# Performance work log

Measured on AMD Instinct MI355X. Metric: run time of the kernel, lower is better.

Reference implementation:

```python
import jax, jax.numpy as jnp
import numpy as np

B, C, H, W = 16, 256, 64, 64
HID, N, SD, NH, HD, NC = 256, 300, 64, 4, 16, 80


def _conv1x1(x, w, b):
    # x: (B,Cin,H,W), w: (Cout,Cin)
    return jnp.einsum('bchw,oc->bohw', x, w) + b[None, :, None, None]


def _lin(x, w, b):
    return x @ w.T + b


def _ln(x, g, b, eps=1e-5):
    mu = x.mean(-1, keepdims=True)
    var = ((x - mu) ** 2).mean(-1, keepdims=True)
    return (x - mu) / jnp.sqrt(var + eps) * g + b


def setup_inputs() -> dict:
    key = jax.random.key(0)
    ks = jax.random.split(key, 16)
    def w(k, shape, s=0.02):
        return jax.random.normal(k, shape, jnp.float32) * s
    return {
        'x': jax.random.normal(ks[0], (B, C, H, W), jnp.float32),
        'spotlight_sources': w(ks[1], (N, SD)),
        'pos_w': w(ks[2], (HID // 2, 2)), 'pos_b': jnp.zeros((HID // 2,), jnp.float32),
        'fp_w': w(ks[3], (HID, C)), 'fp_b': jnp.zeros((HID,), jnp.float32),
        'bn_g': jnp.ones((HID,), jnp.float32), 'bn_b': jnp.zeros((HID,), jnp.float32),
        'bn_m': jnp.zeros((HID,), jnp.float32), 'bn_v': jnp.ones((HID,), jnp.float32),
        'key_w': w(ks[4], (SD, HID)), 'key_b': jnp.zeros((SD,), jnp.float32),
        'val_w': w(ks[5], (HID, HID)), 'val_b': jnp.zeros((HID,), jnp.float32),
        'ctp_w': w(ks[6], (NC, HID)), 'ctp_b': jnp.zeros((NC,), jnp.float32),
        'bb1_w': w(ks[7], (HID, HID)), 'bb1_b': jnp.zeros((HID,), jnp.float32),
        'bbln_g': jnp.ones((HID,), jnp.float32), 'bbln_b': jnp.zeros((HID,), jnp.float32),
        'bb2_w': w(ks[8], (HID // 2, HID)), 'bb2_b': jnp.zeros((HID // 2,), jnp.float32),
        'bb3_w': w(ks[9], (4, HID // 2)), 'bb3_b': jnp.zeros((4,), jnp.float32),
        'ch1_w': w(ks[10], (HID, HID)), 'ch1_b': jnp.zeros((HID,), jnp.float32),
        'chln_g': jnp.ones((HID,), jnp.float32), 'chln_b': jnp.zeros((HID,), jnp.float32),
        'ch2_w': w(ks[11], (HID // 2, HID)), 'ch2_b': jnp.zeros((HID // 2,), jnp.float32),
        'ch3_w': w(ks[12], (1, HID // 2)), 'ch3_b': jnp.zeros((1,), jnp.float32),
    }


def _forward(x, spotlight_sources, pos_w, pos_b, fp_w, fp_b, bn_g, bn_b, bn_m, bn_v,
             key_w, key_b, val_w, val_b, ctp_w, ctp_b,
             bb1_w, bb1_b, bbln_g, bbln_b, bb2_w, bb2_b, bb3_w, bb3_b,
             ch1_w, ch1_b, chln_g, chln_b, ch2_w, ch2_b, ch3_w, ch3_b):
    Bv, _, Hh, Ww = x.shape
    # position encoding: 2-channel normalized (y, x) grid, conv1x1 to HID//2
    y = jnp.linspace(-1.0, 1.0, Hh, dtype=jnp.float32)
    xc = jnp.linspace(-1.0, 1.0, Ww, dtype=jnp.float32)
    coords = jnp.stack([jnp.broadcast_to(y[:, None], (Hh, Ww)),
                        jnp.broadcast_to(xc[None, :], (Hh, Ww))], 0)[None]  # (1,2,H,W)
    # feature_proj: conv1x1 + BatchNorm(eval) + ReLU
    feats = _conv1x1(x, fp_w, fp_b)
    feats = (feats - bn_m[None, :, None, None]) / jnp.sqrt(bn_v[None, :, None, None] + 1e-5)
    feats = jax.nn.relu(feats * bn_g[None, :, None, None] + bn_b[None, :, None, None])
    pos = jnp.broadcast_to(_conv1x1(coords, pos_w, pos_b), (Bv, HID // 2, Hh, Ww))
    comb = jnp.concatenate([feats[:, :HID // 2], pos], axis=1)  # (B,HID,H,W)
    keys = _conv1x1(comb, key_w, key_b).reshape(Bv, NH, HD, Hh * Ww)   # (B,h,d,M)
    vals = _conv1x1(comb, val_w, val_b).reshape(Bv, HID, Hh * Ww)      # (B,HID,M)
    q = spotlight_sources.reshape(N, NH, HD)                            # (N,h,d)
    logits = jnp.einsum('nhd,bhdm->bhnm', q, keys) / jnp.sqrt(jnp.float32(HD))
    attn = jax.nn.softmax(logits, axis=-1).mean(axis=1)                 # (B,N,M), head-averaged
    maps = attn.reshape(Bv, N, Hh, Ww)
    sf = jnp.einsum('bnm,bcm->bnc', attn, vals)                         # (B,N,HID)
    def head(z, w1, b1, g, bb, w2, b2, w3, b3):
        z = jax.nn.relu(_ln(_lin(z, w1, b1), g, bb))
        z = jax.nn.relu(_lin(z, w2, b2))
        return _lin(z, w3, b3)
    boxes = head(sf, bb1_w, bb1_b, bbln_g, bbln_b, bb2_w, bb2_b, bb3_w, bb3_b)
    scores = jax.nn.sigmoid(head(sf, ch1_w, ch1_b, chln_g, chln_b, ch2_w, ch2_b, ch3_w, ch3_b))
    cls = _lin(sf, ctp_w, ctp_b)
    # diversity loss: mean off-diagonal cosine similarity of attention rows
    an = attn / jnp.maximum(jnp.linalg.norm(attn, axis=2, keepdims=True), 1e-12)
    sim = jnp.einsum('bnm,bkm->bnk', an, an)
    div = (sim.sum() - jnp.einsum('bnn->', sim)) / (N * (N - 1)) * 0.1
    return boxes, scores, cls, maps, div, sf


def reference(x, spotlight_sources, pos_w, pos_b, fp_w, fp_b, bn_g, bn_b, bn_m, bn_v,
              key_w, key_b, val_w, val_b, ctp_w, ctp_b,
              bb1_w, bb1_b, bbln_g, bbln_b, bb2_w, bb2_b, bb3_w, bb3_b,
              ch1_w, ch1_b, chln_g, chln_b, ch2_w, ch2_b, ch3_w, ch3_b):
    return _forward(x, spotlight_sources, pos_w, pos_b, fp_w, fp_b, bn_g, bn_b, bn_m, bn_v,
                    key_w, key_b, val_w, val_b, ctp_w, ctp_b,
                    bb1_w, bb1_b, bbln_g, bbln_b, bb2_w, bb2_b, bb3_w, bb3_b,
                    ch1_w, ch1_b, chln_g, chln_b, ch2_w, ch2_b, ch3_w, ch3_b)
```

## Files before the change

kernel.cpp:

```cpp
#include <hip/hip_runtime.h>
#include <math.h>

#define BB 16
#define CIN 256
#define MM 4096
#define HIDC 256
#define NQ 300
#define NHH 4
#define HDD 16

#define OFF_BOXES  0
#define OFF_SCORES 19200
#define OFF_CLS    24000
#define OFF_MAPS   408000
#define OFF_DIV    20068800
#define OFF_SF     20068801

#define WS_COMB16  0
#define WS_KEYS16  8388608
#define WS_ATTN16  10485760
#define WS_T32     20316160
#define WS_T16     21544960
#define WS_VALW16  22159360
#define WS_SUMS    22192128
#define WS_NORM    22211328
#define WS_ACC     22216128
#define WS_P       22216192

#define HP_SF16   (WS_P + 0)
#define HP_Z1PRE  (WS_P + 614400)
#define HP_Z1_16  (WS_P + 1843200)
#define HP_Z2BB   (WS_P + 2457600)
#define HP_Z2CH   (WS_P + 2764800)
#define HP_HW     (WS_P + 3072000)
#define WS_Q16    (WS_P + 3200000)

#define HW_BB1 0
#define HW_CH1 65536
#define HW_BB2 131072
#define HW_CH2 163840
#define HW_CTP 196608

typedef short short8 __attribute__((ext_vector_type(8)));
typedef float floatx4 __attribute__((ext_vector_type(4)));

__device__ __forceinline__ unsigned short f2bf(float f){
  unsigned int u = __float_as_uint(f);
  u = (u + 0x7FFFu + ((u >> 16) & 1u)) >> 16;
  return (unsigned short)u;
}
__device__ __forceinline__ float bf1(unsigned short u){
  return __uint_as_float((unsigned int)u << 16);
}
__device__ __forceinline__ float4 ld_bf4(const unsigned short* p){
  ushort4 u = *(const ushort4*)p;
  float4 f;
  f.x = bf1(u.x); f.y = bf1(u.y); f.z = bf1(u.z); f.w = bf1(u.w);
  return f;
}

__global__ void zero_kernel(float* p){ p[0] = 0.f; }

__global__ __launch_bounds__(256) void zero4_kernel(float4* __restrict__ p, int n4){
  int i = blockIdx.x * 256 + threadIdx.x;
  if (i < n4) p[i] = make_float4(0.f, 0.f, 0.f, 0.f);
}

__global__ __launch_bounds__(256) void cast4_bf16_kernel(const float* __restrict__ src,
                                                         unsigned short* __restrict__ dst, int n4){
  int i = blockIdx.x * 256 + threadIdx.x;
  if (i < n4){
    float4 v = ((const float4*)src)[i];
    ushort4 u;
    u.x = f2bf(v.x); u.y = f2bf(v.y); u.z = f2bf(v.z); u.w = f2bf(v.w);
    ((ushort4*)dst)[i] = u;
  }
}

__global__ __launch_bounds__(256) void castq_kernel(const float* __restrict__ ss,
                                                    unsigned short* __restrict__ q16){
  int i = blockIdx.x * 256 + threadIdx.x;
  if (i < 320*64)
    q16[i] = (i < NQ*64) ? f2bf(ss[i] * 0.25f) : (unsigned short)0;
}

__global__ __launch_bounds__(256) void cast_heads_kernel(
    const float* __restrict__ val_w, const float* __restrict__ bb1_w,
    const float* __restrict__ ch1_w, const float* __restrict__ bb2_w,
    const float* __restrict__ ch2_w, const float* __restrict__ ctp_w,
    unsigned short* __restrict__ valw16, unsigned short* __restrict__ hw16){
  int i = blockIdx.x * 256 + threadIdx.x;
  int T = gridDim.x * 256;
  for (int j = i; j < 65536; j += T) valw16[j] = f2bf(val_w[j]);
  for (int j = i; j < 65536; j += T) hw16[HW_BB1 + j] = f2bf(bb1_w[j]);
  for (int j = i; j < 65536; j += T) hw16[HW_CH1 + j] = f2bf(ch1_w[j]);
  for (int j = i; j < 32768; j += T) hw16[HW_BB2 + j] = f2bf(bb2_w[j]);
  for (int j = i; j < 32768; j += T) hw16[HW_CH2 + j] = f2bf(ch2_w[j]);
  for (int j = i; j < 20480; j += T) hw16[HW_CTP + j] = f2bf(ctp_w[j]);
}

__global__ __launch_bounds__(256) void pos_fill_kernel(const float* __restrict__ pos_w,
                                                       const float* __restrict__ pos_b,
                                                       unsigned short* __restrict__ comb16){
  int idx = blockIdx.x * 256 + threadIdx.x;
  int c = idx >> 12;
  int m = idx & 4095;
  int row = m >> 6, col = m & 63;
  float y = -1.f + 2.f * (float)row / 63.f;
  float x = -1.f + 2.f * (float)col / 63.f;
  unsigned short v = f2bf(pos_w[c*2] * y + pos_w[c*2+1] * x + pos_b[c]);
  #pragma unroll
  for (int b = 0; b < BB; b++)
    comb16[((size_t)(b*HIDC + 128 + c))*MM + m] = v;
}

__global__ __launch_bounds__(256) void comb_gemm_kernel(const float* __restrict__ x,
    const float* __restrict__ fp_w, const float* __restrict__ fp_b,
    const float* __restrict__ bn_g, const float* __restrict__ bn_b,
    const float* __restrict__ bn_m, const float* __restrict__ bn_v,
    unsigned short* __restrict__ comb16){
  int b = blockIdx.z;
  int col0 = blockIdx.x * 128;
  const float* xb = x + (size_t)b * CIN * MM;
  unsigned short* cb = comb16 + (size_t)b * HIDC * MM;
  __shared__ float as[16][132];
  __shared__ float bs[16][128];
  int tx = threadIdx.x, ty = threadIdx.y;
  int tid = ty * 16 + tx;
  float acc[8][8] = {};
  for (int k0 = 0; k0 < CIN; k0 += 16){
    {
      int r = tid >> 1, kh = (tid & 1) * 8;
      float4 v0 = *(const float4*)&fp_w[(size_t)r * CIN + k0 + kh];
      float4 v1 = *(const float4*)&fp_w[(size_t)r * CIN + k0 + kh + 4];
      as[kh+0][r] = v0.x; as[kh+1][r] = v0.y; as[kh+2][r] = v0.z; as[kh+3][r] = v0.w;
      as[kh+4][r] = v1.x; as[kh+5][r] = v1.y; as[kh+6][r] = v1.z; as[kh+7][r] = v1.w;
    }
    {
      int kk = tid >> 4, j = (tid & 15) * 8;
      *(float4*)&bs[kk][j]     = *(const float4*)&xb[(size_t)(k0 + kk) * MM + col0 + j];
      *(float4*)&bs[kk][j + 4] = *(const float4*)&xb[(size_t)(k0 + kk) * MM + col0 + j + 4];
    }
    __syncthreads();
    #pragma unroll
    for (int kk = 0; kk < 16; kk++){
      float4 a0 = *(const float4*)&as[kk][ty*8];
      float4 a1 = *(const float4*)&as[kk][ty*8 + 4];
      float4 b0 = *(const float4*)&bs[kk][tx*8];
      float4 b1 = *(const float4*)&bs[kk][tx*8 + 4];
      float av[8] = {a0.x,a0.y,a0.z,a0.w,a1.x,a1.y,a1.z,a1.w};
      float bv[8] = {b0.x,b0.y,b0.z,b0.w,b1.x,b1.y,b1.z,b1.w};
      #pragma unroll
      for (int i = 0; i < 8; i++)
        #pragma unroll
        for (int j = 0; j < 8; j++)
          acc[i][j] += av[i] * bv[j];
    }
    __syncthreads();
  }
  #pragma unroll
  for (int i = 0; i < 8; i++){
    int r = ty*8 + i;
    float sc = rsqrtf(bn_v[r] + 1e-5f);
    float bias = fp_b[r], mu = bn_m[r], g = bn_g[r], bt = bn_b[r];
    ushort4 o0, o1;
    float v;
    v = fmaxf((acc[i][0] + bias - mu) * sc * g + bt, 0.f); o0.x = f2bf(v);
    v = fmaxf((acc[i][1] + bias - mu) * sc * g + bt, 0.f); o0.y = f2bf(v);
    v = fmaxf((acc[i][2] + bias - mu) * sc * g + bt, 0.f); o0.z = f2bf(v);
    v = fmaxf((acc[i][3] + bias - mu) * sc * g + bt, 0.f); o0.w = f2bf(v);
    v = fmaxf((acc[i][4] + bias - mu) * sc * g + bt, 0.f); o1.x = f2bf(v);
    v = fmaxf((acc[i][5] + bias - mu) * sc * g + bt, 0.f); o1.y = f2bf(v);
    v = fmaxf((acc[i][6] + bias - mu) * sc * g + bt, 0.f); o1.z = f2bf(v);
    v = fmaxf((acc[i][7] + bias - mu) * sc * g + bt, 0.f); o1.w = f2bf(v);
    *(ushort4*)&cb[(size_t)r * MM + col0 + tx*8]     = o0;
    *(ushort4*)&cb[(size_t)r * MM + col0 + tx*8 + 4] = o1;
  }
}

__global__ __launch_bounds__(256) void keys_gemm_kernel(const unsigned short* __restrict__ comb16,
    const float* __restrict__ key_w, const float* __restrict__ key_b,
    unsigned short* __restrict__ keysT){
  int b = blockIdx.z;
  int col0 = blockIdx.x * 128;
  const unsigned short* cb = comb16 + (size_t)b * HIDC * MM;
  unsigned short* kbT = keysT + (size_t)b * MM * 64;
  __shared__ float as[16][68];
  __shared__ float bs[16][132];
  int tx = threadIdx.x, ty = threadIdx.y;
  int tid = ty * 16 + tx;
  float acc[4][8] = {};
  for (int k0 = 0; k0 < HIDC; k0 += 16){
    {
      int r = tid >> 2, kh = (tid & 3) * 4;
      float4 v0 = *(const float4*)&key_w[(size_t)r * HIDC + k0 + kh];
      as[kh+0][r] = v0.x; as[kh+1][r] = v0.y; as[kh+2][r] = v0.z; as[kh+3][r] = v0.w;
    }
    {
      int kk = tid >> 4, j = (tid & 15) * 8;
      float4 f0 = ld_bf4(&cb[(size_t)(k0 + kk) * MM + col0 + j]);
      float4 f1 = ld_bf4(&cb[(size_t)(k0 + kk) * MM + col0 + j + 4]);
      *(float4*)&bs[kk][j]     = f0;
      *(float4*)&bs[kk][j + 4] = f1;
    }
    __syncthreads();
    #pragma unroll
    for (int kk = 0; kk < 16; kk++){
      float4 a0 = *(const float4*)&as[kk][ty*4];
      float4 b0 = *(const float4*)&bs[kk][tx*8];
      float4 b1 = *(const float4*)&bs[kk][tx*8 + 4];
      float av[4] = {a0.x,a0.y,a0.z,a0.w};
      float bv[8] = {b0.x,b0.y,b0.z,b0.w,b1.x,b1.y,b1.z,b1.w};
      #pragma unroll
      for (int i = 0; i < 4; i++)
        #pragma unroll
        for (int j = 0; j < 8; j++)
          acc[i][j] += av[i] * bv[j];
    }
    __syncthreads();
  }
  float kb0 = key_b[ty*4+0], kb1 = key_b[ty*4+1], kb2 = key_b[ty*4+2], kb3 = key_b[ty*4+3];
  #pragma unroll
  for (int j = 0; j < 8; j++){
    int m = col0 + tx*8 + j;
    ushort4 o;
    o.x = f2bf(acc[0][j] + kb0);
    o.y = f2bf(acc[1][j] + kb1);
    o.z = f2bf(acc[2][j] + kb2);
    o.w = f2bf(acc[3][j] + kb3);
    *(ushort4*)&kbT[(size_t)m*64 + ty*4] = o;
  }
}


__global__ __launch_bounds__(256) void attn_sums_kernel(
    const unsigned short* __restrict__ q16, const unsigned short* __restrict__ keysT,
    float* __restrict__ sums){
  int b = blockIdx.z, ny = blockIdx.y, mx = blockIdx.x;
  int tid = threadIdx.x, w = tid >> 6, lane = tid & 63;
  int n0 = ny * 64;
  int l15 = lane & 15, qh = lane >> 4;
  int ko = (qh & 1) * 8;
  bool lo = lane < 32;
  const unsigned short* kT = keysT + (size_t)b * MM * 64;
  int mwb = mx*512 + w*128;
  __shared__ float spart[4][NHH][64];
  short8 zz = {0,0,0,0,0,0,0,0};
  for (int h = 0; h < NHH; h++){
    short8 a[4];
    #pragma unroll
    for (int i = 0; i < 4; i++)
      a[i] = lo ? *(const short8*)&q16[(size_t)(n0 + i*16 + l15)*64 + h*16 + ko] : zz;
    floatx4 sacc[4];
    #pragma unroll
    for (int i = 0; i < 4; i++) sacc[i] = (floatx4){0.f,0.f,0.f,0.f};
    for (int ms = 0; ms < 8; ms++){
      int m = mwb + ms*16 + l15;
      short8 bf = lo ? *(const short8*)&kT[(size_t)m*64 + h*16 + ko] : zz;
      #pragma unroll
      for (int i = 0; i < 4; i++){
        floatx4 l = __builtin_amdgcn_mfma_f32_16x16x32_bf16(a[i], bf,
                        (floatx4){0.f,0.f,0.f,0.f}, 0, 0, 0);
        sacc[i][0] += __expf(l[0]); sacc[i][1] += __expf(l[1]);
        sacc[i][2] += __expf(l[2]); sacc[i][3] += __expf(l[3]);
      }
    }
    #pragma unroll
    for (int i = 0; i < 4; i++)
      #pragma unroll
      for (int reg = 0; reg < 4; reg++){
        float v = sacc[i][reg];
        v += __shfl_xor(v, 1); v += __shfl_xor(v, 2);
        v += __shfl_xor(v, 4); v += __shfl_xor(v, 8);
        if (l15 == 0) spart[w][h][i*16 + qh*4 + reg] = v;
      }
  }
  __syncthreads();
  if (tid < NHH*64){
    int h = tid >> 6, r = tid & 63, n = n0 + r;
    if (n < NQ){
      float v = spart[0][h][r] + spart[1][h][r] + spart[2][h][r] + spart[3][h][r];
      atomicAdd(&sums[((size_t)b*NHH + h)*NQ + n], v);
    }
  }
}

__global__ __launch_bounds__(256) void attn_emit_kernel(
    const unsigned short* __restrict__ q16, const unsigned short* __restrict__ keysT,
    const float* __restrict__ sums, float* __restrict__ maps,
    unsigned short* __restrict__ attn16, float* __restrict__ norms){
  int b = blockIdx.z, ny = blockIdx.y, mx = blockIdx.x;
  int tid = threadIdx.x, w = tid >> 6, lane = tid & 63;
  int n0 = ny * 64;
  int l15 = lane & 15, qh = lane >> 4;
  int ko = (qh & 1) * 8;
  int rq = qh * 4;
  bool lo = lane < 32;
  __shared__ __align__(16) float inv_s[NHH][64];
  __shared__ float npart[4][64];
  if (tid < NHH*64){
    int h = tid >> 6, r = tid & 63, n = n0 + r;
    inv_s[h][r] = (n < NQ) ? 0.25f / sums[((size_t)b*NHH + h)*NQ + n] : 0.f;
  }
  __syncthreads();
  const unsigned short* kT = keysT + (size_t)b * MM * 64;
  int mwb = mx*512 + w*128;
  short8 zz = {0,0,0,0,0,0,0,0};
  short8 a[NHH][4];
  #pragma unroll
  for (int h = 0; h < NHH; h++)
    #pragma unroll
    for (int i = 0; i < 4; i++)
      a[h][i] = lo ? *(const short8*)&q16[(size_t)(n0 + i*16 + l15)*64 + h*16 + ko] : zz;
  floatx4 nacc[4];
  #pragma unroll
  for (int i = 0; i < 4; i++) nacc[i] = (floatx4){0.f,0.f,0.f,0.f};
  float* mb = maps + (size_t)b * NQ * MM;
  unsigned short* ab = attn16 + (size_t)b * NQ * MM;
  for (int ms = 0; ms < 8; ms++){
    int m = mwb + ms*16 + l15;
    floatx4 o[4];
    #pragma unroll
    for (int i = 0; i < 4; i++) o[i] = (floatx4){0.f,0.f,0.f,0.f};
    #pragma unroll
    for (int h = 0; h < NHH; h++){
      short8 bf = lo ? *(const short8*)&kT[(size_t)m*64 + h*16 + ko] : zz;
      #pragma unroll
      for (int i = 0; i < 4; i++){
        floatx4 l = __builtin_amdgcn_mfma_f32_16x16x32_bf16(a[h][i], bf,
                        (floatx4){0.f,0.f,0.f,0.f}, 0, 0, 0);
        floatx4 iv = *(const floatx4*)&inv_s[h][i*16 + rq];
        o[i][0] += __expf(l[0]) * iv[0];
        o[i][1] += __expf(l[1]) * iv[1];
        o[i][2] += __expf(l[2]) * iv[2];
        o[i][3] += __expf(l[3]) * iv[3];
      }
    }
    #pragma unroll
    for (int i = 0; i < 4; i++){
      nacc[i][0] += o[i][0]*o[i][0]; nacc[i][1] += o[i][1]*o[i][1];
      nacc[i][2] += o[i][2]*o[i][2]; nacc[i][3] += o[i][3]*o[i][3];
      #pragma unroll
      for (int reg = 0; reg < 4; reg++){
        int n = n0 + i*16 + rq + reg;
        if (n < NQ){
          mb[(size_t)n*MM + m] = o[i][reg];
          ab[(size_t)n*MM + m] = f2bf(o[i][reg]);
        }
      }
    }
  }
  #pragma unroll
  for (int i = 0; i < 4; i++)
    #pragma unroll
    for (int reg = 0; reg < 4; reg++){
      float v = nacc[i][reg];
      v += __shfl_xor(v, 1); v += __shfl_xor(v, 2);
      v += __shfl_xor(v, 4); v += __shfl_xor(v, 8);
      if (l15 == 0) npart[w][i*16 + rq + reg] = v;
    }
  __syncthreads();
  if (tid < 64){
    int n = n0 + tid;
    if (n < NQ){
      float v = npart[0][tid] + npart[1][tid] + npart[2][tid] + npart[3][tid];
      atomicAdd(&norms[(size_t)b*NQ + n], v);
    }
  }
}

template<bool RELU>
__global__ __launch_bounds__(64) void mfma_nt_kernel(
    const unsigned short* __restrict__ A, size_t sA,
    const unsigned short* __restrict__ B, size_t sB,
    const float* __restrict__ bias,
    float* __restrict__ C, unsigned short* __restrict__ C16,
    size_t sC, int ldc, int Mr, int Nc, int K){
  int bz = blockIdx.z;
  const unsigned short* Ab = A + (size_t)bz * sA;
  const unsigned short* Bb = B + (size_t)bz * sB;
  int lane = threadIdx.x;
  int r16 = lane & 15;
  int ko  = (lane >> 4) * 8;
  const unsigned short* arow[4];
  const unsigned short* brow[4];
  #pragma unroll
  for (int i = 0; i < 4; i++){
    int m = blockIdx.y*64 + i*16 + r16;
    if (m > Mr - 1) m = Mr - 1;
    arow[i] = Ab + (size_t)m * K + ko;
    int n = blockIdx.x*64 + i*16 + r16;
    if (n > Nc - 1) n = Nc - 1;
    brow[i] = Bb + (size_t)n * K + ko;
  }
  floatx4 acc[4][4];
  #pragma unroll
  for (int i = 0; i < 4; i++)
    #pragma unroll
    for (int j = 0; j < 4; j++)
      acc[i][j] = (floatx4){0.f, 0.f, 0.f, 0.f};
  short8 a[4], bv[4], a2[4], b2[4];
  #pragma unroll
  for (int i = 0; i < 4; i++){
    a[i]  = *(const short8*)(arow[i]);
    bv[i] = *(const short8*)(brow[i]);
  }
  for (int k = 32; k < K; k += 32){
    #pragma unroll
    for (int i = 0; i < 4; i++){
      a2[i] = *(const short8*)(arow[i] + k);
      b2[i] = *(const short8*)(brow[i] + k);
    }
    #pragma unroll
    for (int i = 0; i < 4; i++)
      #pragma unroll
      for (int j = 0; j < 4; j++)
        acc[i][j] = __builtin_amdgcn_mfma_f32_16x16x32_bf16(a[i], bv[j], acc[i][j], 0, 0, 0);
    #pragma unroll
    for (int i = 0; i < 4; i++){ a[i] = a2[i]; bv[i] = b2[i]; }
  }
  #pragma unroll
  for (int i = 0; i < 4; i++)
    #pragma unroll
    for (int j = 0; j < 4; j++)
      acc[i][j] = __builtin_amdgcn_mfma_f32_16x16x32_bf16(a[i], bv[j], acc[i][j], 0, 0, 0);
  int cq = lane & 15, rq = (lane >> 4) * 4;
  #pragma unroll
  for (int j = 0; j < 4; j++){
    int cc = blockIdx.x*64 + j*16 + cq;
    if (cc >= Nc) continue;
    float bv_ = bias ? bias[cc] : 0.f;
    #pragma unroll
    for (int i = 0; i < 4; i++){
      int rbase = blockIdx.y*64 + i*16 + rq;
      #pragma unroll
      for (int reg = 0; reg < 4; reg++){
        int rr = rbase + reg;
        if (rr < Mr){
          float v = acc[i][j][reg] + bv_;
          if (RELU) v = fmaxf(v, 0.f);
          size_t o = (size_t)bz * sC + (size_t)rr * ldc + cc;
          if (C)   C[o] = v;
          if (C16) C16[o] = f2bf(v);
        }
      }
    }
  }
}

__global__ __launch_bounds__(64) void mfma_nt_splitk_kernel(
    const unsigned short* __restrict__ A, size_t sA,
    const unsigned short* __restrict__ B, size_t sB,
    float* __restrict__ C, size_t sC, int ldc, int Mr, int K, int kchunk){
  int nks = K / kchunk;
  int bz = blockIdx.z / nks;
  int kz = blockIdx.z % nks;
  const unsigned short* Ab = A + (size_t)bz * sA + (size_t)kz * kchunk;
  const unsigned short* Bb = B + (size_t)bz * sB + (size_t)kz * kchunk;
  int lane = threadIdx.x;
  int r16 = lane & 15;
  int ko  = (lane >> 4) * 8;
  const unsigned short* arow[4];
  const unsigned short* brow[4];
  #pragma unroll
  for (int i = 0; i < 4; i++){
    int m = blockIdx.y*64 + i*16 + r16;
    if (m > Mr - 1) m = Mr - 1;
    arow[i] = Ab + (size_t)m * K + ko;
    int n = blockIdx.x*64 + i*16 + r16;
    brow[i] = Bb + (size_t)n * K + ko;
  }
  floatx4 acc[4][4];
  #pragma unroll
  for (int i = 0; i < 4; i++)
    #pragma unroll
    for (int j = 0; j < 4; j++)
      acc[i][j] = (floatx4){0.f, 0.f, 0.f, 0.f};
  short8 a[4], bv[4], a2[4], b2[4];
  #pragma unroll
  for (int i = 0; i < 4; i++){
    a[i]  = *(const short8*)(arow[i]);
    bv[i] = *(const short8*)(brow[i]);
  }
  for (int k = 32; k < kchunk; k += 32){
    #pragma unroll
    for (int i = 0; i < 4; i++){
      a2[i] = *(const short8*)(arow[i] + k);
      b2[i] = *(const short8*)(brow[i] + k);
    }
    #pragma unroll
    for (int i = 0; i < 4; i++)
      #pragma unroll
      for (int j = 0; j < 4; j++)
        acc[i][j] = __builtin_amdgcn_mfma_f32_16x16x32_bf16(a[i], bv[j], acc[i][j], 0, 0, 0);
    #pragma unroll
    for (int i = 0; i < 4; i++){ a[i] = a2[i]; bv[i] = b2[i]; }
  }
  #pragma unroll
  for (int i = 0; i < 4; i++)
    #pragma unroll
    for (int j = 0; j < 4; j++)
      acc[i][j] = __builtin_amdgcn_mfma_f32_16x16x32_bf16(a[i], bv[j], acc[i][j], 0, 0, 0);
  int cq = lane & 15, rq = (lane >> 4) * 4;
  #pragma unroll
  for (int j = 0; j < 4; j++){
    int cc = blockIdx.x*64 + j*16 + cq;
    #pragma unroll
    for (int i = 0; i < 4; i++){
      int rbase = blockIdx.y*64 + i*16 + rq;
      #pragma unroll
      for (int reg = 0; reg < 4; reg++){
        int rr = rbase + reg;
        if (rr < Mr)
          atomicAdd(&C[(size_t)bz * sC + (size_t)rr * ldc + cc], acc[i][j][reg]);
      }
    }
  }
}

__global__ __launch_bounds__(256) void ln_relu_kernel(const float* __restrict__ zin,
    const float* __restrict__ g, const float* __restrict__ bvec,
    unsigned short* __restrict__ zout){
  int row = blockIdx.x * 4 + (threadIdx.x >> 6);
  int lane = threadIdx.x & 63;
  float4 v = *(const float4*)&zin[(size_t)row * 256 + lane * 4];
  float s = v.x + v.y + v.z + v.w;
  #pragma unroll
  for (int off = 32; off >= 1; off >>= 1) s += __shfl_xor(s, off);
  float mean = s * (1.f/256.f);
  float dx = v.x - mean, dy = v.y - mean, dz = v.z - mean, dw = v.w - mean;
  float sq = dx*dx + dy*dy + dz*dz + dw*dw;
  #pragma unroll
  for (int off = 32; off >= 1; off >>= 1) sq += __shfl_xor(sq, off);
  float inv = rsqrtf(sq * (1.f/256.f) + 1e-5f);
  float4 gv = *(const float4*)&g[lane * 4];
  float4 bb = *(const float4*)&bvec[lane * 4];
  ushort4 u;
  u.x = f2bf(fmaxf(dx*inv*gv.x + bb.x, 0.f));
  u.y = f2bf(fmaxf(dy*inv*gv.y + bb.y, 0.f));
  u.z = f2bf(fmaxf(dz*inv*gv.z + bb.z, 0.f));
  u.w = f2bf(fmaxf(dw*inv*gv.w + bb.w, 0.f));
  *(ushort4*)&zout[(size_t)row * 256 + lane * 4] = u;
}

__global__ __launch_bounds__(256) void head3_kernel(
    const unsigned short* __restrict__ z2bb, const unsigned short* __restrict__ z2ch,
    const float* __restrict__ bb3_w, const float* __restrict__ bb3_b,
    const float* __restrict__ ch3_w, const float* __restrict__ ch3_b,
    float* __restrict__ boxes, float* __restrict__ scores){
  int row = blockIdx.x * 4 + (threadIdx.x >> 6);
  int lane = threadIdx.x & 63;
  float zb0 = bf1(z2bb[(size_t)row*128 + 2*lane]);
  float zb1 = bf1(z2bb[(size_t)row*128 + 2*lane + 1]);
  float zc0 = bf1(z2ch[(size_t)row*128 + 2*lane]);
  float zc1 = bf1(z2ch[(size_t)row*128 + 2*lane + 1]);
  float acc[5];
  #pragma unroll
  for (int o = 0; o < 4; o++)
    acc[o] = bb3_w[o*128 + 2*lane]*zb0 + bb3_w[o*128 + 2*lane + 1]*zb1;
  acc[4] = ch3_w[2*lane]*zc0 + ch3_w[2*lane + 1]*zc1;
  #pragma unroll
  for (int o = 0; o < 5; o++){
    float v = acc[o];
    #pragma unroll
    for (int off = 32; off >= 1; off >>= 1) v += __shfl_xor(v, off);
    acc[o] = v;
  }
  if (lane == 0){
    #pragma unroll
    for (int o = 0; o < 4; o++)
      boxes[(size_t)row*4 + o] = acc[o] + bb3_b[o];
    float sv = acc[4] + ch3_b[0];
    scores[row] = 1.f / (1.f + __expf(-sv));
  }
}

__global__ __launch_bounds__(256) void simdiv_kernel(const unsigned short* __restrict__ attn16,
    const float* __restrict__ norms, float* __restrict__ acc){
  int b = blockIdx.y;
  int m = blockIdx.x * 256 + threadIdx.x;
  __shared__ float inv_s[NQ];
  __shared__ float red[4];
  for (int i = threadIdx.x; i < NQ; i += 256)
    inv_s[i] = 1.f / fmaxf(sqrtf(norms[(size_t)b * NQ + i]), 1e-12f);
  __syncthreads();
  const unsigned short* ab = attn16 + (size_t)b * NQ * MM;
  float S = 0.f;
  for (int n = 0; n < NQ; n++)
    S += bf1(ab[(size_t)n * MM + m]) * inv_s[n];
  float p = S * S;
  #pragma unroll
  for (int off = 32; off >= 1; off >>= 1) p += __shfl_xor(p, off);
  int w = threadIdx.x >> 6, lane = threadIdx.x & 63;
  if (lane == 0) red[w] = p;
  __syncthreads();
  if (threadIdx.x == 0) atomicAdd(acc, red[0] + red[1] + red[2] + red[3]);
}

__global__ void finalize_kernel(const float* __restrict__ acc, float* __restrict__ out_div){
  out_div[0] = (acc[0] - (float)(BB * NQ)) / (float)(NQ * (NQ - 1)) * 0.1f;
}

extern "C" void kernel_launch(void* const* d_in, const int* in_sizes, int n_in,
                              void* d_out, int out_size, void* d_ws, size_t ws_size,
                              hipStream_t stream){
  const float* x      = (const float*)d_in[0];
  const float* ss     = (const float*)d_in[1];
  const float* pos_w  = (const float*)d_in[2];
  const float* pos_b  = (const float*)d_in[3];
  const float* fp_w   = (const float*)d_in[4];
  const float* fp_b   = (const float*)d_in[5];
  const float* bn_g   = (const float*)d_in[6];
  const float* bn_b   = (const float*)d_in[7];
  const float* bn_m   = (const float*)d_in[8];
  const float* bn_v   = (const float*)d_in[9];
  const float* key_w  = (const float*)d_in[10];
  const float* key_b  = (const float*)d_in[11];
  const float* val_w  = (const float*)d_in[12];
  const float* val_b  = (const float*)d_in[13];
  const float* ctp_w  = (const float*)d_in[14];
  const float* ctp_b  = (const float*)d_in[15];
  const float* bb1_w  = (const float*)d_in[16];
  const float* bb1_b  = (const float*)d_in[17];
  const float* bbln_g = (const float*)d_in[18];
  const float* bbln_b = (const float*)d_in[19];
  const float* bb2_w  = (const float*)d_in[20];
  const float* bb2_b  = (const float*)d_in[21];
  const float* bb3_w  = (const float*)d_in[22];
  const float* bb3_b  = (const float*)d_in[23];
  const float* ch1_w  = (const float*)d_in[24];
  const float* ch1_b  = (const float*)d_in[25];
  const float* chln_g = (const float*)d_in[26];
  const float* chln_b = (const float*)d_in[27];
  const float* ch2_w  = (const float*)d_in[28];
  const float* ch2_b  = (const float*)d_in[29];
  const float* ch3_w  = (const float*)d_in[30];
  const float* ch3_b  = (const float*)d_in[31];

  float* out    = (float*)d_out;
  float* boxes  = out + OFF_BOXES;
  float* scores = out + OFF_SCORES;
  float* cls    = out + OFF_CLS;
  float* maps   = out + OFF_MAPS;
  float* divp   = out + OFF_DIV;
  float* sfout  = out + OFF_SF;

  float* ws = (float*)d_ws;
  unsigned short* comb16 = (unsigned short*)(ws + WS_COMB16);
  unsigned short* keysT  = (unsigned short*)(ws + WS_KEYS16);
  unsigned short* attn16 = (unsigned short*)(ws + WS_ATTN16);
  float*          t32    = ws + WS_T32;
  unsigned short* t16    = (unsigned short*)(ws + WS_T16);
  unsigned short* valw16 = (unsigned short*)(ws + WS_VALW16);
  float* sums  = ws + WS_SUMS;
  float* norms = ws + WS_NORM;
  float* dacc  = ws + WS_ACC;
  unsigned short* sf16   = (unsigned short*)(ws + HP_SF16);
  float*          z1pre  = ws + HP_Z1PRE;
  unsigned short* z1_16  = (unsigned short*)(ws + HP_Z1_16);
  unsigned short* z2bb16 = (unsigned short*)(ws + HP_Z2BB);
  unsigned short* z2ch16 = (unsigned short*)(ws + HP_Z2CH);
  unsigned short* hw16   = (unsigned short*)(ws + HP_HW);
  unsigned short* q16    = (unsigned short*)(ws + WS_Q16);

  zero_kernel<<<1, 1, 0, stream>>>(dacc);
  zero4_kernel<<<1200, 256, 0, stream>>>((float4*)t32, 307200);
  zero4_kernel<<<24, 256, 0, stream>>>((float4*)sums, 6000);
  castq_kernel<<<80, 256, 0, stream>>>(ss, q16);
  pos_fill_kernel<<<2048, 256, 0, stream>>>(pos_w, pos_b, comb16);
  comb_gemm_kernel<<<dim3(32,1,16), dim3(16,16), 0, stream>>>(x, fp_w, fp_b, bn_g, bn_b, bn_m, bn_v, comb16);
  keys_gemm_kernel<<<dim3(32,1,16), dim3(16,16), 0, stream>>>(comb16, key_w, key_b, keysT);

  attn_sums_kernel<<<dim3(8,5,16), 256, 0, stream>>>(q16, keysT, sums);
  attn_emit_kernel<<<dim3(8,5,16), 256, 0, stream>>>(q16, keysT, sums, maps, attn16, norms);

  mfma_nt_splitk_kernel<<<dim3(4,5,BB*4), 64, 0, stream>>>(
      attn16, (size_t)NQ*MM, comb16, (size_t)HIDC*MM,
      t32, (size_t)NQ*HIDC, HIDC, NQ, MM, MM/4);
  cast4_bf16_kernel<<<1200, 256, 0, stream>>>(t32, t16, 307200);
  cast_heads_kernel<<<256, 256, 0, stream>>>(val_w, bb1_w, ch1_w, bb2_w, ch2_w, ctp_w, valw16, hw16);
  mfma_nt_kernel<false><<<dim3(4,5,BB), 64, 0, stream>>>(
      t16, (size_t)NQ*HIDC, valw16, 0, val_b,
      sfout, sf16, (size_t)NQ*HIDC, HIDC, NQ, HIDC, HIDC);

  mfma_nt_kernel<false><<<dim3(4,75,1), 64, 0, stream>>>(
      sf16, 0, hw16 + HW_BB1, 0, bb1_b, z1pre, nullptr, 0, 256, 4800, 256, 256);
  ln_relu_kernel<<<1200, 256, 0, stream>>>(z1pre, bbln_g, bbln_b, z1_16);
  mfma_nt_kernel<true><<<dim3(2,75,1), 64, 0, stream>>>(
      z1_16, 0, hw16 + HW_BB2, 0, bb2_b, nullptr, z2bb16, 0, 128, 4800, 128, 256);
  mfma_nt_kernel<false><<<dim3(4,75,1), 64, 0, stream>>>(
      sf16, 0, hw16 + HW_CH1, 0, ch1_b, z1pre, nullptr, 0, 256, 4800, 256, 256);
  ln_relu_kernel<<<1200, 256, 0, stream>>>(z1pre, chln_g, chln_b, z1_16);
  mfma_nt_kernel<true><<<dim3(2,75,1), 64, 0, stream>>>(
      z1_16, 0, hw16 + HW_CH2, 0, ch2_b, nullptr, z2ch16, 0, 128, 4800, 128, 256);
  head3_kernel<<<1200, 256, 0, stream>>>(z2bb16, z2ch16, bb3_w, bb3_b, ch3_w, ch3_b, boxes, scores);
  mfma_nt_kernel<false><<<dim3(2,75,1), 64, 0, stream>>>(
      sf16, 0, hw16 + HW_CTP, 0, ctp_b, cls, nullptr, 0, 80, 4800, 80, 256);

  simdiv_kernel<<<dim3(16,16), 256, 0, stream>>>(attn16, norms, dacc);
  finalize_kernel<<<1, 1, 0, stream>>>(dacc, divp);
}
```

Baseline: 556.3 us.

## Move feature projection and key GEMMs to bf16 MFMA with transposed inputs

Replaces the fp32 FMA tiled GEMMs for the 1x1 conv projection and the key projection with bf16 MFMA kernels. Inputs are first cast to bf16 and transposed into K-contiguous layouts (x to xT16, comb16 to combT), and the weights are cast to bf16 once. The aim is to cut the compute cost of the two largest dense GEMMs by using matrix cores. In exchange it adds two transpose passes with extra global traffic, rounds x to bf16 before the conv, and writes the comb output with scattered 2-byte stores.

New measurement: 565.2 us. Within noise of the previous version (+1.6%).

```diff
diff --git a/kernel.cpp b/kernel.cpp
--- a/kernel.cpp
+++ b/kernel.cpp
@@ -34,6 +34,10 @@
 #define HP_Z2CH   (WS_P + 2764800)
 #define HP_HW     (WS_P + 3072000)
 #define WS_Q16    (WS_P + 3200000)
+#define WS_XT     25426432
+#define WS_COMBT  33815040
+#define WS_FPW16  42203648
+#define WS_KEYW16 42220032
 
 #define HW_BB1 0
 #define HW_CH1 65536
@@ -51,12 +55,6 @@
 }
 __device__ __forceinline__ float bf1(unsigned short u){
   return __uint_as_float((unsigned int)u << 16);
-}
-__device__ __forceinline__ float4 ld_bf4(const unsigned short* p){
-  ushort4 u = *(const ushort4*)p;
-  float4 f;
-  f.x = bf1(u.x); f.y = bf1(u.y); f.z = bf1(u.z); f.w = bf1(u.w);
-  return f;
 }
 
 __global__ void zero_kernel(float* p){ p[0] = 0.f; }
@@ -82,6 +80,14 @@
   int i = blockIdx.x * 256 + threadIdx.x;
   if (i < 320*64)
     q16[i] = (i < NQ*64) ? f2bf(ss[i] * 0.25f) : (unsigned short)0;
+}
+
+__global__ __launch_bounds__(256) void cast_w2_kernel(const float* __restrict__ fp_w,
+    const float* __restrict__ key_w,
+    unsigned short* __restrict__ fpw16, unsigned short* __restrict__ keyw16){
+  int i = blockIdx.x * 256 + threadIdx.x;
+  if (i < 128*256) fpw16[i] = f2bf(fp_w[i]);
+  if (i < 64*256)  keyw16[i] = f2bf(key_w[i]);
 }
 
 __global__ __launch_bounds__(256) void cast_heads_kernel(
@@ -114,121 +120,118 @@
     comb16[((size_t)(b*HIDC + 128 + c))*MM + m] = v;
 }
 
-__global__ __launch_bounds__(256) void comb_gemm_kernel(const float* __restrict__ x,
-    const float* __restrict__ fp_w, const float* __restrict__ fp_b,
-    const float* __restrict__ bn_g, const float* __restrict__ bn_b,
-    const float* __restrict__ bn_m, const float* __restrict__ bn_v,
-    unsigned short* __restrict__ comb16){
+template<bool INF32>
+__global__ __launch_bounds__(256) void transpose_kernel(
+    const void* __restrict__ in, unsigned short* __restrict__ outp){
   int b = blockIdx.z;
-  int col0 = blockIdx.x * 128;
-  const float* xb = x + (size_t)b * CIN * MM;
+  int m0 = blockIdx.x * 64;
+  int r0 = blockIdx.y * 64;
+  __shared__ unsigned short lds[64][65];
+  int t = threadIdx.x;
+  if (INF32){
+    const float* ib = (const float*)in + (size_t)b * CIN * MM;
+    #pragma unroll
+    for (int j = 0; j < 4; j++){
+      int lin = j*256 + t;
+      int rr = lin >> 4;
+      int m4 = (lin & 15) * 4;
+      float4 v = *(const float4*)&ib[(size_t)(r0 + rr)*MM + m0 + m4];
+      lds[m4+0][rr] = f2bf(v.x);
+      lds[m4+1][rr] = f2bf(v.y);
+      lds[m4+2][rr] = f2bf(v.z);
+      lds[m4+3][rr] = f2bf(v.w);
+    }
+  } else {
+    const unsigned short* ib = (const unsigned short*)in + (size_t)b * CIN * MM;
+    #pragma unroll
+    for (int j = 0; j < 4; j++){
+      int lin = j*256 + t;
+      int rr = lin >> 4;
+      int m4 = (lin & 15) * 4;
+      ushort4 v = *(const ushort4*)&ib[(size_t)(r0 + rr)*MM + m0 + m4];
+      lds[m4+0][rr] = v.x; lds[m4+1][rr] = v.y;
+      lds[m4+2][rr] = v.z; lds[m4+3][rr] = v.w;
+    }
+  }
+  __syncthreads();
+  unsigned short* ob = outp + (size_t)b * MM * CIN;
+  #pragma unroll
+  for (int j = 0; j < 4; j++){
+    int lin = j*256 + t;
+    int mm = lin >> 4;
+    int c4 = (lin & 15) * 4;
+    ushort4 u;
+    u.x = lds[mm][c4+0]; u.y = lds[mm][c4+1];
+    u.z = lds[mm][c4+2]; u.w = lds[mm][c4+3];
+    *(ushort4*)&ob[(size_t)(m0 + mm)*CIN + r0 + c4] = u;
+  }
+}
+
+__global__ __launch_bounds__(64) void comb_mfma_kernel(
+    const unsigned short* __restrict__ fpw16, const unsigned short* __restrict__ xT16,
+    const float* __restrict__ fp_b, const float* __restrict__ bn_g,
+    const float* __restrict__ bn_b, const float* __restrict__ bn_m,
+    const float* __restrict__ bn_v, unsigned short* __restrict__ comb16){
+  int b = blockIdx.z;
+  const unsigned short* Bb = xT16 + (size_t)b * MM * CIN;
   unsigned short* cb = comb16 + (size_t)b * HIDC * MM;
-  __shared__ float as[16][132];
-  __shared__ float bs[16][128];
-  int tx = threadIdx.x, ty = threadIdx.y;
-  int tid = ty * 16 + tx;
-  float acc[8][8] = {};
-  for (int k0 = 0; k0 < CIN; k0 += 16){
-    {
-      int r = tid >> 1, kh = (tid & 1) * 8;
-      float4 v0 = *(const float4*)&fp_w[(size_t)r * CIN + k0 + kh];
-      float4 v1 = *(const float4*)&fp_w[(size_t)r * CIN + k0 + kh + 4];
-      as[kh+0][r] = v0.x; as[kh+1][r] = v0.y; as[kh+2][r] = v0.z; as[kh+3][r] = v0.w;
-      as[kh+4][r] = v1.x; as[kh+5][r] = v1.y; as[kh+6][r] = v1.z; as[kh+7][r] = v1.w;
-    }
-    {
-      int kk = tid >> 4, j = (tid & 15) * 8;
-      *(float4*)&bs[kk][j]     = *(const float4*)&xb[(size_t)(k0 + kk) * MM + col0 + j];
-      *(float4*)&bs[kk][j + 4] = *(const float4*)&xb[(size_t)(k0 + kk) * MM + col0 + j + 4];
-    }
-    __syncthreads();
-    #pragma unroll
-    for (int kk = 0; kk < 16; kk++){
-      float4 a0 = *(const float4*)&as[kk][ty*8];
-      float4 a1 = *(const float4*)&as[kk][ty*8 + 4];
-      float4 b0 = *(const float4*)&bs[kk][tx*8];
-      float4 b1 = *(const float4*)&bs[kk][tx*8 + 4];
-      float av[8] = {a0.x,a0.y,a0.z,a0.w,a1.x,a1.y,a1.z,a1.w};
-      float bv[8] = {b0.x,b0.y,b0.z,b0.w,b1.x,b1.y,b1.z,b1.w};
-      #pragma unroll
-      for (int i = 0; i < 8; i++)
-        #pragma unroll
-        for (int j = 0; j < 8; j++)
-          acc[i][j] += av[i] * bv[j];
-    }
-    __syncthreads();
-  }
-  #pragma unroll
-  for (int i = 0; i < 8; i++){
-    int r = ty*8 + i;
-    float sc = rsqrtf(bn_v[r] + 1e-5f);
-    float bias = fp_b[r], mu = bn_m[r], g = bn_g[r], bt = bn_b[r];
-    ushort4 o0, o1;
-    float v;
-    v = fmaxf((acc[i][0] + bias - mu) * sc * g + bt, 0.f); o0.x = f2bf(v);
-    v = fmaxf((acc[i][1] + bias - mu) * sc * g + bt, 0.f); o0.y = f2bf(v);
-    v = fmaxf((acc[i][2] + bias - mu) * sc * g + bt, 0.f); o0.z = f2bf(v);
-    v = fmaxf((acc[i][3] + bias - mu) * sc * g + bt, 0.f); o0.w = f2bf(v);
-    v = fmaxf((acc[i][4] + bias - mu) * sc * g + bt, 0.f); o1.x = f2bf(v);
-    v = fmaxf((acc[i][5] + bias - mu) * sc * g + bt, 0.f); o1.y = f2bf(v);
-    v = fmaxf((acc[i][6] + bias - mu) * sc * g + bt, 0.f); o1.z = f2bf(v);
-    v = fmaxf((acc[i][7] + bias - mu) * sc * g + bt, 0.f); o1.w = f2bf(v);
-    *(ushort4*)&cb[(size_t)r * MM + col0 + tx*8]     = o0;
-    *(ushort4*)&cb[(size_t)r * MM + col0 + tx*8 + 4] = o1;
-  }
-}
-
-__global__ __launch_bounds__(256) void keys_gemm_kernel(const unsigned short* __restrict__ comb16,
-    const float* __restrict__ key_w, const float* __restrict__ key_b,
-    unsigned short* __restrict__ keysT){
-  int b = blockIdx.z;
-  int col0 = blockIdx.x * 128;
-  const unsigned short* cb = comb16 + (size_t)b * HIDC * MM;
-  unsigned short* kbT = keysT + (size_t)b * MM * 64;
-  __shared__ float as[16][68];
-  __shared__ float bs[16][132];
-  int tx = threadIdx.x, ty = threadIdx.y;
-  int tid = ty * 16 + tx;
-  float acc[4][8] = {};
-  for (int k0 = 0; k0 < HIDC; k0 += 16){
-    {
-      int r = tid >> 2, kh = (tid & 3) * 4;
-      float4 v0 = *(const float4*)&key_w[(size_t)r * HIDC + k0 + kh];
-      as[kh+0][r] = v0.x; as[kh+1][r] = v0.y; as[kh+2][r] = v0.z; as[kh+3][r] = v0.w;
-    }
-    {
-      int kk = tid >> 4, j = (tid & 15) * 8;
-      float4 f0 = ld_bf4(&cb[(size_t)(k0 + kk) * MM + col0 + j]);
-      float4 f1 = ld_bf4(&cb[(size_t)(k0 + kk) * MM + col0 + j + 4]);
-      *(float4*)&bs[kk][j]     = f0;
-      *(float4*)&bs[kk][j + 4] = f1;
-    }
-    __syncthreads();
-    #pragma unroll
-    for (int kk = 0; kk < 16; kk++){
-      float4 a0 = *(const float4*)&as[kk][ty*4];
-      float4 b0 = *(const float4*)&bs[kk][tx*8];
-      float4 b1 = *(const float4*)&bs[kk][tx*8 + 4];
-      float av[4] = {a0.x,a0.y,a0.z,a0.w};
-      float bv[8] = {b0.x,b0.y,b0.z,b0.w,b1.x,b1.y,b1.z,b1.w};
-      #pragma unroll
-      for (int i = 0; i < 4; i++)
-        #pragma unroll
-        for (int j = 0; j < 8; j++)
-          acc[i][j] += av[i] * bv[j];
-    }
-    __syncthreads();
-  }
-  float kb0 = key_b[ty*4+0], kb1 = key_b[ty*4+1], kb2 = key_b[ty*4+2], kb3 = key_b[ty*4+3];
-  #pragma unroll
-  for (int j = 0; j < 8; j++){
-    int m = col0 + tx*8 + j;
-    ushort4 o;
-    o.x = f2bf(acc[0][j] + kb0);
-    o.y = f2bf(acc[1][j] + kb1);
-    o.z = f2bf(acc[2][j] + kb2);
-    o.w = f2bf(acc[3][j] + kb3);
-    *(ushort4*)&kbT[(size_t)m*64 + ty*4] = o;
+  int lane = threadIdx.x;
+  int r16 = lane & 15;
+  int ko  = (lane >> 4) * 8;
+  const unsigned short* arow[4];
+  const unsigned short* brow[4];
+  #pragma unroll
+  for (int i = 0; i < 4; i++){
+    arow[i] = fpw16 + (size_t)(blockIdx.y*64 + i*16 + r16) * CIN + ko;
+    brow[i] = Bb + (size_t)(blockIdx.x*64 + i*16 + r16) * CIN + ko;
+  }
+  floatx4 acc[4][4];
+  #pragma unroll
+  for (int i = 0; i < 4; i++)
+    #pragma unroll
+    for (int j = 0; j < 4; j++)
+      acc[i][j] = (floatx4){0.f, 0.f, 0.f, 0.f};
+  short8 a[4], bv[4], a2[4], b2[4];
+  #pragma unroll
+  for (int i = 0; i < 4; i++){
+    a[i]  = *(const short8*)(arow[i]);
+    bv[i] = *(const short8*)(brow[i]);
+  }
+  for (int k = 32; k < CIN; k += 32){
+    #pragma unroll
+    for (int i = 0; i < 4; i++){
+      a2[i] = *(const short8*)(arow[i] + k);
+      b2[i] = *(const short8*)(brow[i] + k);
+    }
+    #pragma unroll
+    for (int i = 0; i < 4; i++)
+      #pragma unroll
+      for (int j = 0; j < 4; j++)
+        acc[i][j] = __builtin_amdgcn_mfma_f32_16x16x32_bf16(a[i], bv[j], acc[i][j], 0, 0, 0);
+    #pragma unroll
+    for (int i = 0; i < 4; i++){ a[i] = a2[i]; bv[i] = b2[i]; }
+  }
+  #pragma unroll
+  for (int i = 0; i < 4; i++)
+    #pragma unroll
+    for (int j = 0; j < 4; j++)
+      acc[i][j] = __builtin_amdgcn_mfma_f32_16x16x32_bf16(a[i], bv[j], acc[i][j], 0, 0, 0);
+  int cq = lane & 15, rq = (lane >> 4) * 4;
+  #pragma unroll
+  for (int i = 0; i < 4; i++){
+    #pragma unroll
+    for (int reg = 0; reg < 4; reg++){
+      int rr = blockIdx.y*64 + i*16 + rq + reg;
+      float sc  = rsqrtf(bn_v[rr] + 1e-5f);
+      float mul = sc * bn_g[rr];
+      float ofs = (fp_b[rr] - bn_m[rr]) * mul + bn_b[rr];
+      #pragma unroll
+      for (int j = 0; j < 4; j++){
+        int cc = blockIdx.x*64 + j*16 + cq;
+        float v = fmaxf(acc[i][j][reg] * mul + ofs, 0.f);
+        cb[(size_t)rr * MM + cc] = f2bf(v);
+      }
+    }
   }
 }
 
@@ -662,14 +665,25 @@
   unsigned short* z2ch16 = (unsigned short*)(ws + HP_Z2CH);
   unsigned short* hw16   = (unsigned short*)(ws + HP_HW);
   unsigned short* q16    = (unsigned short*)(ws + WS_Q16);
+  unsigned short* xT16   = (unsigned short*)(ws + WS_XT);
+  unsigned short* combT  = (unsigned short*)(ws + WS_COMBT);
+  unsigned short* fpw16  = (unsigned short*)(ws + WS_FPW16);
+  unsigned short* keyw16 = (unsigned short*)(ws + WS_KEYW16);
 
   zero_kernel<<<1, 1, 0, stream>>>(dacc);
   zero4_kernel<<<1200, 256, 0, stream>>>((float4*)t32, 307200);
   zero4_kernel<<<24, 256, 0, stream>>>((float4*)sums, 6000);
   castq_kernel<<<80, 256, 0, stream>>>(ss, q16);
+  cast_w2_kernel<<<128, 256, 0, stream>>>(fp_w, key_w, fpw16, keyw16);
+
+  transpose_kernel<true><<<dim3(64,4,16), 256, 0, stream>>>(x, xT16);
   pos_fill_kernel<<<2048, 256, 0, stream>>>(pos_w, pos_b, comb16);
-  comb_gemm_kernel<<<dim3(32,1,16), dim3(16,16), 0, stream>>>(x, fp_w, fp_b, bn_g, bn_b, bn_m, bn_v, comb16);
-  keys_gemm_kernel<<<dim3(32,1,16), dim3(16,16), 0, stream>>>(comb16, key_w, key_b, keysT);
+  comb_mfma_kernel<<<dim3(64,2,16), 64, 0, stream>>>(
+      fpw16, xT16, fp_b, bn_g, bn_b, bn_m, bn_v, comb16);
+  transpose_kernel<false><<<dim3(64,4,16), 256, 0, stream>>>(comb16, combT);
+  mfma_nt_kernel<false><<<dim3(1,64,16), 64, 0, stream>>>(
+      combT, (size_t)MM*CIN, keyw16, 0, key_b,
+      nullptr, keysT, (size_t)MM*64, 64, MM, 64, CIN);
 
   attn_sums_kernel<<<dim3(8,5,16), 256, 0, stream>>>(q16, keysT, sums);
   attn_emit_kernel<<<dim3(8,5,16), 256, 0, stream>>>(q16, keysT, sums, maps, attn16, norms);
```
